# Kernel optimization log

Measured on AMD Instinct MI355X. Metric: run time of the kernel, lower is better.

Reference implementation:

```python
import jax, jax.numpy as jnp
import numpy as np

C = jnp.complex64

# Hadamard gate
_HG = jnp.asarray(np.array([[1.0, 1.0], [1.0, -1.0]]) / np.sqrt(2.0), dtype=C)


def _rx(angles):
    # angles: [P] -> batched RX gates [P, 2, 2]
    c = jnp.cos(angles / 2).astype(C)
    s = (-1j * jnp.sin(angles / 2)).astype(C)
    return jnp.stack([jnp.stack([c, s], -1), jnp.stack([s, c], -1)], -2)


def _x_theta(theta):
    # X_theta_gate with cos(pi/2)=0, sin(pi/2)=1:
    # [[0, -i e^{i t/2}], [-i e^{-i t/2}, 0]]
    e = jnp.exp(0.5j * theta.astype(C))
    z = jnp.zeros((), C)
    row0 = jnp.stack([z, -1j * e])
    row1 = jnp.stack([-1j * jnp.conj(e), z])
    return jnp.stack([row0, row1])


def _cu(theta):
    # controlled-U as rank-4 tensor CU[c_out, t_out, c_in, t_in]
    cu = jnp.zeros((2, 2, 2, 2), C)
    cu = cu.at[0, :, 0, :].set(jnp.eye(2, dtype=C))
    cu = cu.at[1, :, 1, :].set(_x_theta(theta))
    return cu

# state axes: p (patch), a..e = wires 0..4
_RX_SPECS = ['pij,pajcde->paicde', 'pij,pabjde->pabide',
             'pij,pabcje->pabcie', 'pij,pabcdj->pabcdi']
# controlled gates: (ctrl1,tgt2), (ctrl2,tgt3), (ctrl3,tgt4), (ctrl4,tgt1)
_CU_SPECS = ['ijkl,paklde->paijde', 'ijkl,pabkle->pabije',
             'ijkl,pabckl->pabcij', 'ijkl,palcdk->pajcdi']


def _simulate(pix, thetas, phis):
    # pix: [P, 12] per-patch angles; returns <Z_0> per patch, [P]
    P = pix.shape[0]
    s = jnp.zeros((P, 2, 2, 2, 2, 2), C).at[:, 0, 0, 0, 0, 0].set(1.0)
    s = jnp.einsum('ij,pjbcde->pibcde', _HG, s)  # H on wire 0
    for layer in range(3):
        for w in range(4):
            g = _rx(pix[:, 4 * layer + w])
            s = jnp.einsum(_RX_SPECS[w], g, s)
        for w in range(4):
            cu = _cu(thetas[4 * layer + w])
            s = jnp.einsum(_CU_SPECS[w], cu, s)
        # CPhase(phi) on wires [0, 1]
        phase = jnp.ones((2, 2), C).at[1, 1].set(jnp.exp(1j * phis[layer].astype(C)))
        s = s * phase[None, :, :, None, None, None]
    s = jnp.einsum('ij,pjbcde->pibcde', _HG, s)  # final H on wire 0
    sign = jnp.array([1.0, -1.0], jnp.float32)
    probs = jnp.abs(s) ** 2
    return jnp.sum(probs * sign[None, :, None, None, None, None], axis=(1, 2, 3, 4, 5))


def setup_inputs() -> dict:
    key = jax.random.key(0)
    k1, k2, k3 = jax.random.split(key, 3)
    x = jax.random.normal(k1, (16, 3, 256, 256), dtype=jnp.float32)
    thetas = jax.random.normal(k2, (12,), dtype=jnp.float32)
    phis = jax.random.normal(k3, (3,), dtype=jnp.float32)
    return {'x': x, 'thetas': thetas, 'phis': phis}


def reference(x, thetas, phis):
    B, Cch, H, W = x.shape
    H2, W2 = H // 2, W // 2
    # extract 2x2 patches: order per patch = [(0,0),(0,1),(1,0),(1,1)] per channel
    pix = x.reshape(B, 3, H2, 2, W2, 2).transpose(0, 2, 4, 1, 3, 5).reshape(B * H2 * W2, 12)
    ev = _simulate(pix, thetas, phis)  # [P]
    return ev.reshape(B, 1, H2, W2).astype(jnp.float32)
```

## Files before the change

### kernel.cpp

```cpp
#include <hip/hip_runtime.h>


__device__ __forceinline__ void sc_half(float ang, float& s, float& c) {
    const float r = ang * 0.07957747154594767f;
    s = __builtin_amdgcn_sinf(r);
    c = __builtin_amdgcn_cosf(r);
}
__device__ __forceinline__ void sc_full(float ang, float& s, float& c) {
    const float r = ang * 0.15915494309189535f;
    s = __builtin_amdgcn_sinf(r);
    c = __builtin_amdgcn_cosf(r);
}

template<int BIT>
__device__ __forceinline__ void apply_rx(float (&sr)[32], float (&si)[32],
                                         float c, float s) {
#pragma unroll
    for (int m = 0; m < 16; ++m) {
        const int lo = m & ((1 << BIT) - 1);
        const int hi = (m >> BIT) << (BIT + 1);
        const int i0 = hi | lo;
        const int i1 = i0 | (1 << BIT);
        const float ar = sr[i0], ai = si[i0];
        const float br = sr[i1], bi = si[i1];
        sr[i0] = c * ar + s * bi;
        si[i0] = c * ai - s * br;
        sr[i1] = s * ai + c * br;
        si[i1] = c * bi - s * ar;
    }
}

template<int CBIT, int TBIT>
__device__ __forceinline__ void apply_cu(float (&sr)[32], float (&si)[32],
                                         float u01r, float u01i,
                                         float u10r, float u10i) {
#pragma unroll
    for (int m = 0; m < 16; ++m) {
        const int lo = m & ((1 << TBIT) - 1);
        const int hi = (m >> TBIT) << (TBIT + 1);
        const int i0 = hi | lo;
        if (!(i0 & (1 << CBIT))) continue;
        const int i1 = i0 | (1 << TBIT);
        const float ar = sr[i0], ai = si[i0];
        const float br = sr[i1], bi = si[i1];
        sr[i0] = u01r * br - u01i * bi;
        si[i0] = u01r * bi + u01i * br;
        sr[i1] = u10r * ar - u10i * ai;
        si[i1] = u10r * ai + u10i * ar;
    }
}

__global__ __launch_bounds__(256)
void qsim_kernel(const float* __restrict__ x,
                 const float* __restrict__ thetas,
                 const float* __restrict__ phis,
                 float* __restrict__ out, int P) {
    const int p = blockIdx.x * blockDim.x + threadIdx.x;
    if (p >= P) return;

    const int b   = p >> 14;
    const int rem = p & 16383;
    const int i   = rem >> 7;
    const int j   = rem & 127;

    float pix[12];
    const float2* __restrict__ x2 = (const float2*)x;
#pragma unroll
    for (int c = 0; c < 3; ++c) {
#pragma unroll
        for (int dy = 0; dy < 2; ++dy) {
            const long row = ((long)(b * 3 + c) * 256 + (2 * i + dy));
            const float2 v = x2[row * 128 + j];
            pix[c * 4 + dy * 2 + 0] = v.x;
            pix[c * 4 + dy * 2 + 1] = v.y;
        }
    }

    float sr[32], si[32];
    {
        float s1, c1, s2, c2, s3, c3, s4, c4;
        sc_half(pix[0], s1, c1);
        sc_half(pix[1], s2, c2);
        sc_half(pix[2], s3, c3);
        sc_half(pix[3], s4, c4);
        const float pA[4] = {c1 * c2, c1 * s2, s1 * c2, s1 * s2};
        const float pB[4] = {c3 * c4, c3 * s4, s3 * c4, s3 * s4};
#pragma unroll
        for (int m = 0; m < 16; ++m) {
            const float v = pA[m >> 2] * pB[m & 3];
            const int pc = __builtin_popcount((unsigned)m) & 3;
            sr[m] = (pc == 0) ? v : ((pc == 2) ? -v : 0.f);
            si[m] = (pc == 1) ? -v : ((pc == 3) ? v : 0.f);
        }
#pragma unroll
        for (int m = 0; m < 16; ++m) { sr[m + 16] = sr[m]; si[m + 16] = si[m]; }
    }

#pragma unroll
    for (int L = 0; L < 3; ++L) {
        if (L > 0) {
            float sn, cs;
            sc_half(pix[4 * L + 0], sn, cs); apply_rx<3>(sr, si, cs, sn);
            sc_half(pix[4 * L + 1], sn, cs); apply_rx<2>(sr, si, cs, sn);
            sc_half(pix[4 * L + 2], sn, cs); apply_rx<1>(sr, si, cs, sn);
            sc_half(pix[4 * L + 3], sn, cs); apply_rx<0>(sr, si, cs, sn);
        }
        {
            float sn, cs;
            sc_half(thetas[4 * L + 0], sn, cs);
            apply_cu<3, 2>(sr, si, sn, -cs, -sn, -cs);
            sc_half(thetas[4 * L + 1], sn, cs);
            apply_cu<2, 1>(sr, si, sn, -cs, -sn, -cs);
            sc_half(thetas[4 * L + 2], sn, cs);
            apply_cu<1, 0>(sr, si, sn, -cs, -sn, -cs);
            sc_half(thetas[4 * L + 3], sn, cs);
            apply_cu<0, 3>(sr, si, sn, -cs, -sn, -cs);
        }
        {
            float sn, cs;
            sc_full(phis[L], sn, cs);
#pragma unroll
            for (int m = 24; m < 32; ++m) {
                const float ar = sr[m], ai = si[m];
                sr[m] = cs * ar - sn * ai;
                si[m] = cs * ai + sn * ar;
            }
        }
    }

    float ev = 0.f;
#pragma unroll
    for (int m = 0; m < 16; ++m) {
        ev += sr[m] * sr[m + 16] + si[m] * si[m + 16];
    }
    out[p] = ev;
}

extern "C" void kernel_launch(void* const* d_in, const int* in_sizes, int n_in,
                              void* d_out, int out_size, void* d_ws, size_t ws_size,
                              hipStream_t stream) {
    const float* x      = (const float*)d_in[0];
    const float* thetas = (const float*)d_in[1];
    const float* phis   = (const float*)d_in[2];
    float* out = (float*)d_out;
    const int P = out_size;
    const int threads = 256;
    const int blocks = (P + threads - 1) / threads;
    qsim_kernel<<<blocks, threads, 0, stream>>>(x, thetas, phis, out, P);
}
```

Before: 76.95 us.

## Process two patches per thread with packed FP32 FMA and specialize first layer

```diff
diff --git a/kernel.cpp b/kernel.cpp
--- a/kernel.cpp
+++ b/kernel.cpp
@@ -1,5 +1,19 @@
 #include <hip/hip_runtime.h>
 
+
+typedef float f2 __attribute__((ext_vector_type(2)));
+
+__device__ __forceinline__ f2 pk_fma(f2 a, f2 b, f2 c) {
+    f2 d;
+    asm("v_pk_fma_f32 %0, %1, %2, %3" : "=v"(d) : "v"(a), "v"(b), "v"(c));
+    return d;
+}
+__device__ __forceinline__ f2 pk_mul(f2 a, f2 b) {
+    f2 d;
+    asm("v_pk_mul_f32 %0, %1, %2" : "=v"(d) : "v"(a), "v"(b));
+    return d;
+}
+__device__ __forceinline__ f2 sp(float v) { f2 r; r.x = v; r.y = v; return r; }
 
 __device__ __forceinline__ void sc_half(float ang, float& s, float& c) {
     const float r = ang * 0.07957747154594767f;
@@ -11,42 +25,49 @@
     s = __builtin_amdgcn_sinf(r);
     c = __builtin_amdgcn_cosf(r);
 }
+__device__ __forceinline__ void sc_half2(f2 ang, f2& s, f2& c) {
+    float s0, c0, s1, c1;
+    sc_half(ang.x, s0, c0);
+    sc_half(ang.y, s1, c1);
+    s.x = s0; s.y = s1; c.x = c0; c.y = c1;
+}
 
 template<int BIT>
-__device__ __forceinline__ void apply_rx(float (&sr)[32], float (&si)[32],
-                                         float c, float s) {
+__device__ __forceinline__ void apply_rx(f2 (&R)[32], f2 (&I)[32],
+                                         f2 c, f2 s, f2 ns) {
 #pragma unroll
     for (int m = 0; m < 16; ++m) {
         const int lo = m & ((1 << BIT) - 1);
         const int hi = (m >> BIT) << (BIT + 1);
         const int i0 = hi | lo;
         const int i1 = i0 | (1 << BIT);
-        const float ar = sr[i0], ai = si[i0];
-        const float br = sr[i1], bi = si[i1];
-        sr[i0] = c * ar + s * bi;
-        si[i0] = c * ai - s * br;
-        sr[i1] = s * ai + c * br;
-        si[i1] = c * bi - s * ar;
+        const f2 ar = R[i0], ai = I[i0];
+        const f2 br = R[i1], bi = I[i1];
+        R[i0] = pk_fma(c, ar, pk_mul(s,  bi));
+        I[i0] = pk_fma(c, ai, pk_mul(ns, br));
+        R[i1] = pk_fma(c, br, pk_mul(s,  ai));
+        I[i1] = pk_fma(c, bi, pk_mul(ns, ar));
     }
 }
 
-template<int CBIT, int TBIT>
-__device__ __forceinline__ void apply_cu(float (&sr)[32], float (&si)[32],
-                                         float u01r, float u01i,
-                                         float u10r, float u10i) {
+template<int CBIT, int TBIT, int NB>
+__device__ __forceinline__ void cu_gate(f2 (&R)[32], f2 (&I)[32],
+                                        float sn, float cs) {
+    const f2 u01r = sp(sn),  u01i = sp(-cs), nu01i = sp(cs);
+    const f2 u10r = sp(-sn), u10i = sp(-cs), nu10i = sp(cs);
 #pragma unroll
-    for (int m = 0; m < 16; ++m) {
+    for (int m = 0; m < NB; ++m) {
         const int lo = m & ((1 << TBIT) - 1);
         const int hi = (m >> TBIT) << (TBIT + 1);
         const int i0 = hi | lo;
         if (!(i0 & (1 << CBIT))) continue;
         const int i1 = i0 | (1 << TBIT);
-        const float ar = sr[i0], ai = si[i0];
-        const float br = sr[i1], bi = si[i1];
-        sr[i0] = u01r * br - u01i * bi;
-        si[i0] = u01r * bi + u01i * br;
-        sr[i1] = u10r * ar - u10i * ai;
-        si[i1] = u10r * ai + u10i * ar;
+        const f2 ar = R[i0], ai = I[i0];
+        const f2 br = R[i1], bi = I[i1];
+        R[i0] = pk_fma(u01r, br, pk_mul(nu01i, bi));
+        I[i0] = pk_fma(u01r, bi, pk_mul(u01i,  br));
+        R[i1] = pk_fma(u10r, ar, pk_mul(nu10i, ai));
+        I[i1] = pk_fma(u10r, ai, pk_mul(u10i,  ar));
     }
 }
 
@@ -55,85 +76,106 @@
                  const float* __restrict__ thetas,
                  const float* __restrict__ phis,
                  float* __restrict__ out, int P) {
-    const int p = blockIdx.x * blockDim.x + threadIdx.x;
-    if (p >= P) return;
+    const int t = blockIdx.x * blockDim.x + threadIdx.x;
+    const int T = P >> 1;
+    if (t >= T) return;
 
-    const int b   = p >> 14;
-    const int rem = p & 16383;
-    const int i   = rem >> 7;
-    const int j   = rem & 127;
+    const int b  = t >> 13;
+    const int i  = (t & 8191) >> 6;
+    const int jt = t & 63;
 
-    float pix[12];
-    const float2* __restrict__ x2 = (const float2*)x;
+    f2 pix[12];
+    const float4* __restrict__ x4 = (const float4*)x;
 #pragma unroll
     for (int c = 0; c < 3; ++c) {
 #pragma unroll
         for (int dy = 0; dy < 2; ++dy) {
             const long row = ((long)(b * 3 + c) * 256 + (2 * i + dy));
-            const float2 v = x2[row * 128 + j];
-            pix[c * 4 + dy * 2 + 0] = v.x;
-            pix[c * 4 + dy * 2 + 1] = v.y;
+            const float4 v = x4[row * 64 + jt];
+            f2 a0; a0.x = v.x; a0.y = v.z;
+            f2 a1; a1.x = v.y; a1.y = v.w;
+            pix[c * 4 + dy * 2 + 0] = a0;
+            pix[c * 4 + dy * 2 + 1] = a1;
         }
     }
 
-    float sr[32], si[32];
+    f2 R[32], I[32];
     {
-        float s1, c1, s2, c2, s3, c3, s4, c4;
-        sc_half(pix[0], s1, c1);
-        sc_half(pix[1], s2, c2);
-        sc_half(pix[2], s3, c3);
-        sc_half(pix[3], s4, c4);
-        const float pA[4] = {c1 * c2, c1 * s2, s1 * c2, s1 * s2};
-        const float pB[4] = {c3 * c4, c3 * s4, s3 * c4, s3 * s4};
+        f2 s1, c1, s2, c2, s3, c3, s4, c4;
+        sc_half2(pix[0], s1, c1);
+        sc_half2(pix[1], s2, c2);
+        sc_half2(pix[2], s3, c3);
+        sc_half2(pix[3], s4, c4);
+        f2 pA[4], pB[4];
+        pA[0] = pk_mul(c1, c2); pA[1] = pk_mul(c1, s2);
+        pA[2] = pk_mul(s1, c2); pA[3] = pk_mul(s1, s2);
+        pB[0] = pk_mul(c3, c4); pB[1] = pk_mul(c3, s4);
+        pB[2] = pk_mul(s3, c4); pB[3] = pk_mul(s3, s4);
 #pragma unroll
         for (int m = 0; m < 16; ++m) {
-            const float v = pA[m >> 2] * pB[m & 3];
+            const f2 v  = pk_mul(pA[m >> 2], pB[m & 3]);
+            const f2 nv = -v;
+            const f2 z  = sp(0.f);
             const int pc = __builtin_popcount((unsigned)m) & 3;
-            sr[m] = (pc == 0) ? v : ((pc == 2) ? -v : 0.f);
-            si[m] = (pc == 1) ? -v : ((pc == 3) ? v : 0.f);
+            R[m] = (pc == 0) ? v  : ((pc == 2) ? nv : z);
+            I[m] = (pc == 1) ? nv : ((pc == 3) ? v  : z);
         }
+    }
+
+    {
+        float sn, cs;
+        sc_half(thetas[0], sn, cs); cu_gate<3, 2, 8>(R, I, sn, cs);
+        sc_half(thetas[1], sn, cs); cu_gate<2, 1, 8>(R, I, sn, cs);
+        sc_half(thetas[2], sn, cs); cu_gate<1, 0, 8>(R, I, sn, cs);
+        sc_half(thetas[3], sn, cs); cu_gate<0, 3, 8>(R, I, sn, cs);
+    }
+    {
+        float snp, csp;
+        sc_full(phis[0], snp, csp);
+        const f2 cp = sp(csp), spp = sp(snp), np = sp(-snp);
 #pragma unroll
-        for (int m = 0; m < 16; ++m) { sr[m + 16] = sr[m]; si[m + 16] = si[m]; }
+        for (int m = 0; m < 8; ++m) { R[m + 16] = R[m]; I[m + 16] = I[m]; }
+#pragma unroll
+        for (int m = 8; m < 16; ++m) {
+            R[m + 16] = pk_fma(cp, R[m], pk_mul(np,  I[m]));
+            I[m + 16] = pk_fma(cp, I[m], pk_mul(spp, R[m]));
+        }
     }
 
 #pragma unroll
-    for (int L = 0; L < 3; ++L) {
-        if (L > 0) {
+    for (int L = 1; L < 3; ++L) {
+        f2 s2v, c2v;
+        sc_half2(pix[4 * L + 0], s2v, c2v); apply_rx<3>(R, I, c2v, s2v, -s2v);
+        sc_half2(pix[4 * L + 1], s2v, c2v); apply_rx<2>(R, I, c2v, s2v, -s2v);
+        sc_half2(pix[4 * L + 2], s2v, c2v); apply_rx<1>(R, I, c2v, s2v, -s2v);
+        sc_half2(pix[4 * L + 3], s2v, c2v); apply_rx<0>(R, I, c2v, s2v, -s2v);
+        {
             float sn, cs;
-            sc_half(pix[4 * L + 0], sn, cs); apply_rx<3>(sr, si, cs, sn);
-            sc_half(pix[4 * L + 1], sn, cs); apply_rx<2>(sr, si, cs, sn);
-            sc_half(pix[4 * L + 2], sn, cs); apply_rx<1>(sr, si, cs, sn);
-            sc_half(pix[4 * L + 3], sn, cs); apply_rx<0>(sr, si, cs, sn);
+            sc_half(thetas[4 * L + 0], sn, cs); cu_gate<3, 2, 16>(R, I, sn, cs);
+            sc_half(thetas[4 * L + 1], sn, cs); cu_gate<2, 1, 16>(R, I, sn, cs);
+            sc_half(thetas[4 * L + 2], sn, cs); cu_gate<1, 0, 16>(R, I, sn, cs);
+            sc_half(thetas[4 * L + 3], sn, cs); cu_gate<0, 3, 16>(R, I, sn, cs);
         }
         {
-            float sn, cs;
-            sc_half(thetas[4 * L + 0], sn, cs);
-            apply_cu<3, 2>(sr, si, sn, -cs, -sn, -cs);
-            sc_half(thetas[4 * L + 1], sn, cs);
-            apply_cu<2, 1>(sr, si, sn, -cs, -sn, -cs);
-            sc_half(thetas[4 * L + 2], sn, cs);
-            apply_cu<1, 0>(sr, si, sn, -cs, -sn, -cs);
-            sc_half(thetas[4 * L + 3], sn, cs);
-            apply_cu<0, 3>(sr, si, sn, -cs, -sn, -cs);
-        }
-        {
-            float sn, cs;
-            sc_full(phis[L], sn, cs);
+            float snp, csp;
+            sc_full(phis[L], snp, csp);
+            const f2 cp = sp(csp), spp = sp(snp), np = sp(-snp);
 #pragma unroll
             for (int m = 24; m < 32; ++m) {
-                const float ar = sr[m], ai = si[m];
-                sr[m] = cs * ar - sn * ai;
-                si[m] = cs * ai + sn * ar;
+                const f2 r = R[m], ii = I[m];
+                R[m] = pk_fma(cp, r,  pk_mul(np,  ii));
+                I[m] = pk_fma(cp, ii, pk_mul(spp, r));
             }
         }
     }
 
-    float ev = 0.f;
+    f2 ev = sp(0.f);
 #pragma unroll
     for (int m = 0; m < 16; ++m) {
-        ev += sr[m] * sr[m + 16] + si[m] * si[m + 16];
+        ev = pk_fma(R[m], R[m + 16], pk_fma(I[m], I[m + 16], ev));
     }
-    out[p] = ev;
+    float2 o; o.x = ev.x; o.y = ev.y;
+    reinterpret_cast<float2*>(out)[t] = o;
 }
 
 extern "C" void kernel_launch(void* const* d_in, const int* in_sizes, int n_in,
@@ -144,7 +186,8 @@
     const float* phis   = (const float*)d_in[2];
     float* out = (float*)d_out;
     const int P = out_size;
+    const int T = P >> 1;
     const int threads = 256;
-    const int blocks = (P + threads - 1) / threads;
+    const int blocks = (T + threads - 1) / threads;
     qsim_kernel<<<blocks, threads, 0, stream>>>(x, thetas, phis, out, P);
 }
```

After: 69.97 us. 9.1% less time.

## Pack wire-0 amplitude pairs into float2 vectors for packed FP32 math

Applied to the files above, without the earlier changes.

```diff
diff --git a/kernel.cpp b/kernel.cpp
--- a/kernel.cpp
+++ b/kernel.cpp
@@ -1,5 +1,7 @@
 #include <hip/hip_runtime.h>
 
+
+typedef float f2 __attribute__((ext_vector_type(2)));
 
 __device__ __forceinline__ void sc_half(float ang, float& s, float& c) {
     const float r = ang * 0.07957747154594767f;
@@ -13,44 +15,54 @@
 }
 
 template<int BIT>
-__device__ __forceinline__ void apply_rx(float (&sr)[32], float (&si)[32],
+__device__ __forceinline__ void apply_rx(f2 (&R)[16], f2 (&I)[16],
                                          float c, float s) {
 #pragma unroll
-    for (int m = 0; m < 16; ++m) {
+    for (int m = 0; m < 8; ++m) {
         const int lo = m & ((1 << BIT) - 1);
         const int hi = (m >> BIT) << (BIT + 1);
         const int i0 = hi | lo;
         const int i1 = i0 | (1 << BIT);
-        const float ar = sr[i0], ai = si[i0];
-        const float br = sr[i1], bi = si[i1];
-        sr[i0] = c * ar + s * bi;
-        si[i0] = c * ai - s * br;
-        sr[i1] = s * ai + c * br;
-        si[i1] = c * bi - s * ar;
+        const f2 ar = R[i0], ai = I[i0];
+        const f2 br = R[i1], bi = I[i1];
+        R[i0] = c * ar + s * bi;
+        I[i0] = c * ai - s * br;
+        R[i1] = c * br + s * ai;
+        I[i1] = c * bi - s * ar;
     }
 }
 
 template<int CBIT, int TBIT>
-__device__ __forceinline__ void apply_cu(float (&sr)[32], float (&si)[32],
-                                         float u01r, float u01i,
-                                         float u10r, float u10i) {
+__device__ __forceinline__ void cu_gate(f2 (&R)[16], f2 (&I)[16],
+                                        float sn, float cs) {
 #pragma unroll
-    for (int m = 0; m < 16; ++m) {
+    for (int m = 0; m < 8; ++m) {
         const int lo = m & ((1 << TBIT) - 1);
         const int hi = (m >> TBIT) << (TBIT + 1);
         const int i0 = hi | lo;
         if (!(i0 & (1 << CBIT))) continue;
         const int i1 = i0 | (1 << TBIT);
-        const float ar = sr[i0], ai = si[i0];
-        const float br = sr[i1], bi = si[i1];
-        sr[i0] = u01r * br - u01i * bi;
-        si[i0] = u01r * bi + u01i * br;
-        sr[i1] = u10r * ar - u10i * ai;
-        si[i1] = u10r * ai + u10i * ar;
+        const f2 ar = R[i0], ai = I[i0];
+        const f2 br = R[i1], bi = I[i1];
+        R[i0] =  sn * br + cs * bi;
+        I[i0] =  sn * bi - cs * br;
+        R[i1] = -sn * ar + cs * ai;
+        I[i1] = -sn * ai - cs * ar;
     }
 }
 
-__global__ __launch_bounds__(256)
+__device__ __forceinline__ void cphase(f2 (&R)[16], f2 (&I)[16],
+                                       float sn, float cs) {
+    const f2 C = {1.f, cs}, S = {0.f, sn};
+#pragma unroll
+    for (int m = 8; m < 16; ++m) {
+        const f2 r = R[m], ii = I[m];
+        R[m] = C * r  - S * ii;
+        I[m] = C * ii + S * r;
+    }
+}
+
+__global__ __launch_bounds__(256, 4)
 void qsim_kernel(const float* __restrict__ x,
                  const float* __restrict__ thetas,
                  const float* __restrict__ phis,
@@ -63,75 +75,95 @@
     const int i   = rem >> 7;
     const int j   = rem & 127;
 
-    float pix[12];
     const float2* __restrict__ x2 = (const float2*)x;
-#pragma unroll
-    for (int c = 0; c < 3; ++c) {
-#pragma unroll
-        for (int dy = 0; dy < 2; ++dy) {
-            const long row = ((long)(b * 3 + c) * 256 + (2 * i + dy));
-            const float2 v = x2[row * 128 + j];
-            pix[c * 4 + dy * 2 + 0] = v.x;
-            pix[c * 4 + dy * 2 + 1] = v.y;
-        }
-    }
+    const long rowbase = (long)b * 768 + 2 * i;
 
-    float sr[32], si[32];
+    float2 v0 = x2[(rowbase + 0) * 128 + j];
+    float2 v1 = x2[(rowbase + 1) * 128 + j];
+
+    f2 R[16], I[16];
     {
         float s1, c1, s2, c2, s3, c3, s4, c4;
-        sc_half(pix[0], s1, c1);
-        sc_half(pix[1], s2, c2);
-        sc_half(pix[2], s3, c3);
-        sc_half(pix[3], s4, c4);
+        sc_half(v0.x, s1, c1);
+        sc_half(v0.y, s2, c2);
+        sc_half(v1.x, s3, c3);
+        sc_half(v1.y, s4, c4);
         const float pA[4] = {c1 * c2, c1 * s2, s1 * c2, s1 * s2};
         const float pB[4] = {c3 * c4, c3 * s4, s3 * c4, s3 * s4};
 #pragma unroll
         for (int m = 0; m < 16; ++m) {
             const float v = pA[m >> 2] * pB[m & 3];
             const int pc = __builtin_popcount((unsigned)m) & 3;
-            sr[m] = (pc == 0) ? v : ((pc == 2) ? -v : 0.f);
-            si[m] = (pc == 1) ? -v : ((pc == 3) ? v : 0.f);
+            const float rr = (pc == 0) ? v : ((pc == 2) ? -v : 0.f);
+            const float ii = (pc == 1) ? -v : ((pc == 3) ? v : 0.f);
+            R[m] = (f2){rr, rr};
+            I[m] = (f2){ii, ii};
         }
-#pragma unroll
-        for (int m = 0; m < 16; ++m) { sr[m + 16] = sr[m]; si[m + 16] = si[m]; }
     }
 
-#pragma unroll
-    for (int L = 0; L < 3; ++L) {
-        if (L > 0) {
-            float sn, cs;
-            sc_half(pix[4 * L + 0], sn, cs); apply_rx<3>(sr, si, cs, sn);
-            sc_half(pix[4 * L + 1], sn, cs); apply_rx<2>(sr, si, cs, sn);
-            sc_half(pix[4 * L + 2], sn, cs); apply_rx<1>(sr, si, cs, sn);
-            sc_half(pix[4 * L + 3], sn, cs); apply_rx<0>(sr, si, cs, sn);
-        }
-        {
-            float sn, cs;
-            sc_half(thetas[4 * L + 0], sn, cs);
-            apply_cu<3, 2>(sr, si, sn, -cs, -sn, -cs);
-            sc_half(thetas[4 * L + 1], sn, cs);
-            apply_cu<2, 1>(sr, si, sn, -cs, -sn, -cs);
-            sc_half(thetas[4 * L + 2], sn, cs);
-            apply_cu<1, 0>(sr, si, sn, -cs, -sn, -cs);
-            sc_half(thetas[4 * L + 3], sn, cs);
-            apply_cu<0, 3>(sr, si, sn, -cs, -sn, -cs);
-        }
-        {
-            float sn, cs;
-            sc_full(phis[L], sn, cs);
-#pragma unroll
-            for (int m = 24; m < 32; ++m) {
-                const float ar = sr[m], ai = si[m];
-                sr[m] = cs * ar - sn * ai;
-                si[m] = cs * ai + sn * ar;
-            }
-        }
+    v0 = x2[(rowbase + 256) * 128 + j];
+    v1 = x2[(rowbase + 257) * 128 + j];
+
+    {
+        float sn, cs;
+        sc_half(thetas[0], sn, cs); cu_gate<3, 2>(R, I, sn, cs);
+        sc_half(thetas[1], sn, cs); cu_gate<2, 1>(R, I, sn, cs);
+        sc_half(thetas[2], sn, cs); cu_gate<1, 0>(R, I, sn, cs);
+        sc_half(thetas[3], sn, cs); cu_gate<0, 3>(R, I, sn, cs);
+    }
+    {
+        float sn, cs;
+        sc_full(phis[0], sn, cs);
+        cphase(R, I, sn, cs);
+    }
+
+    {
+        float sn, cs;
+        sc_half(v0.x, sn, cs); apply_rx<3>(R, I, cs, sn);
+        sc_half(v0.y, sn, cs); apply_rx<2>(R, I, cs, sn);
+        sc_half(v1.x, sn, cs); apply_rx<1>(R, I, cs, sn);
+        sc_half(v1.y, sn, cs); apply_rx<0>(R, I, cs, sn);
+    }
+    v0 = x2[(rowbase + 512) * 128 + j];
+    v1 = x2[(rowbase + 513) * 128 + j];
+
+    {
+        float sn, cs;
+        sc_half(thetas[4], sn, cs); cu_gate<3, 2>(R, I, sn, cs);
+        sc_half(thetas[5], sn, cs); cu_gate<2, 1>(R, I, sn, cs);
+        sc_half(thetas[6], sn, cs); cu_gate<1, 0>(R, I, sn, cs);
+        sc_half(thetas[7], sn, cs); cu_gate<0, 3>(R, I, sn, cs);
+    }
+    {
+        float sn, cs;
+        sc_full(phis[1], sn, cs);
+        cphase(R, I, sn, cs);
+    }
+
+    {
+        float sn, cs;
+        sc_half(v0.x, sn, cs); apply_rx<3>(R, I, cs, sn);
+        sc_half(v0.y, sn, cs); apply_rx<2>(R, I, cs, sn);
+        sc_half(v1.x, sn, cs); apply_rx<1>(R, I, cs, sn);
+        sc_half(v1.y, sn, cs); apply_rx<0>(R, I, cs, sn);
+    }
+    {
+        float sn, cs;
+        sc_half(thetas[ 8], sn, cs); cu_gate<3, 2>(R, I, sn, cs);
+        sc_half(thetas[ 9], sn, cs); cu_gate<2, 1>(R, I, sn, cs);
+        sc_half(thetas[10], sn, cs); cu_gate<1, 0>(R, I, sn, cs);
+        sc_half(thetas[11], sn, cs); cu_gate<0, 3>(R, I, sn, cs);
+    }
+    {
+        float sn, cs;
+        sc_full(phis[2], sn, cs);
+        cphase(R, I, sn, cs);
     }
 
     float ev = 0.f;
 #pragma unroll
     for (int m = 0; m < 16; ++m) {
-        ev += sr[m] * sr[m + 16] + si[m] * si[m + 16];
+        ev += R[m].x * R[m].y + I[m].x * I[m].y;
     }
     out[p] = ev;
 }
```

After: 71.84 us. 1.07x faster.
